# Kernel tuning notes

Hardware: AMD Instinct MI355X
Metric: run time of the kernel (lower is better)

Reference implementation:

```python
import jax, jax.numpy as jnp
import numpy as np

T = 2048
HIDDEN = 4096
NH = 32        # query heads
NKV = 8        # kv heads
G = NH // NKV  # GQA group size
D = 128        # head_dim (== v_head_dim)
ROPE_BASE = 1000000.0


def setup_inputs() -> dict:
    key = jax.random.key(0)
    ks = jax.random.split(key, 8)
    s = 0.02
    return {
        "positions": jnp.arange(T, dtype=jnp.int32),
        "hidden_states": jax.random.normal(ks[0], (T, HIDDEN), dtype=jnp.float32),
        "Wq": jax.random.normal(ks[1], (HIDDEN, NH * D), dtype=jnp.float32) * s,
        "bq": jnp.zeros((NH * D,), dtype=jnp.float32),
        "Wk": jax.random.normal(ks[2], (HIDDEN, NKV * D), dtype=jnp.float32) * s,
        "bk": jnp.zeros((NKV * D,), dtype=jnp.float32),
        "Wv": jax.random.normal(ks[3], (HIDDEN, NKV * D), dtype=jnp.float32) * s,
        "bv": jnp.zeros((NKV * D,), dtype=jnp.float32),
        "Wo": jax.random.normal(ks[4], (NH * D, HIDDEN), dtype=jnp.float32) * s,
    }


def _rope(positions, x):
    # neox-style rotary, full rotary_dim = D
    half = D // 2
    inv_freq = 1.0 / (ROPE_BASE ** (jnp.arange(0, half, dtype=jnp.float32) / half))
    freqs = positions.astype(jnp.float32)[:, None] * inv_freq[None, :]  # [T, half]
    cos = jnp.cos(freqs)[:, None, :]  # [T, 1, half]
    sin = jnp.sin(freqs)[:, None, :]
    x1, x2 = x[..., :half], x[..., half:]
    return jnp.concatenate([x1 * cos - x2 * sin, x2 * cos + x1 * sin], axis=-1)


def reference(positions, hidden_states, Wq, bq, Wk, bk, Wv, bv, Wo):
    q = (hidden_states @ Wq + bq).reshape(T, NH, D)
    k = (hidden_states @ Wk + bk).reshape(T, NKV, D)
    v = (hidden_states @ Wv + bv).reshape(T, NKV, D)
    q = _rope(positions, q)
    k = _rope(positions, k)

    scale = D ** -0.5
    qg = q.reshape(T, NKV, G, D)
    # scores: [NKV, G, T(query), S(key)]
    scores = jnp.einsum("tkgd,skd->kgts", qg, k) * scale
    causal = positions[:, None] >= positions[None, :]  # [T, S]
    scores = jnp.where(causal[None, None, :, :], scores, jnp.finfo(scores.dtype).min)
    probs = jax.nn.softmax(scores, axis=-1)
    attn = jnp.einsum("kgts,skd->tkgd", probs, v).reshape(T, NH * D)

    output = attn @ Wo
    kv_fused = jnp.stack([k, v], axis=0)  # [2, T, NKV, D]
    return output, kv_fused
```

## Files before the change

kernel.cpp:

```cpp
#include <hip/hip_runtime.h>
#include <stdint.h>

#define T_SEQ 2048
#define HIDDEN_DIM 4096
#define NH 32
#define NKV 8
#define HD 128
#define QKV_N 6144

typedef unsigned short u16;
typedef __attribute__((__ext_vector_type__(8))) __bf16 bf16x8;
typedef __attribute__((__ext_vector_type__(4))) float f32x4;

__device__ __forceinline__ float exp2_fast(float x) {
    return __builtin_amdgcn_exp2f(x);
}

__device__ __forceinline__ u16 f2bf(float f) {
    union { float f; unsigned u; } x; x.f = f;
    unsigned u = x.u;
    unsigned r = u + 0x7FFFu + ((u >> 16) & 1u);
    return (u16)(r >> 16);
}
__device__ __forceinline__ float bf2f(u16 h) {
    union { unsigned u; float f; } x; x.u = ((unsigned)h) << 16;
    return x.f;
}

__device__ __forceinline__ void gl_lds16(const u16* g, u16* l) {
    __builtin_amdgcn_global_load_lds((__attribute__((address_space(1))) void*)g,
                                     (__attribute__((address_space(3))) void*)l,
                                     16, 0, 0);
}

#define BAR()                                  \
    {                                          \
        asm volatile("" ::: "memory");         \
        __builtin_amdgcn_s_barrier();          \
        asm volatile("" ::: "memory");         \
    }

__global__ __launch_bounds__(256) void cast_f32_bf16(const float* __restrict__ in,
                                                     u16* __restrict__ out, int n4) {
    int i = blockIdx.x * 256 + threadIdx.x;
    if (i < n4) {
        float4 v = ((const float4*)in)[i];
        uint2 o;
        o.x = (unsigned)f2bf(v.x) | ((unsigned)f2bf(v.y) << 16);
        o.y = (unsigned)f2bf(v.z) | ((unsigned)f2bf(v.w) << 16);
        ((uint2*)out)[i] = o;
    }
}

__global__ __launch_bounds__(256) void transpose_cast(const float* __restrict__ W,
                                                      u16* __restrict__ Wt, int R, int C) {
    __shared__ float tile[32][33];
    int c0 = blockIdx.x * 32, r0 = blockIdx.y * 32;
    int tx = threadIdx.x & 31;
    int ty = threadIdx.x >> 5;
#pragma unroll
    for (int i = 0; i < 32; i += 8)
        tile[ty + i][tx] = W[(size_t)(r0 + ty + i) * C + c0 + tx];
    __syncthreads();
#pragma unroll
    for (int i = 0; i < 32; i += 8)
        Wt[(size_t)(c0 + ty + i) * R + r0 + tx] = f2bf(tile[tx][ty + i]);
}

__global__ __launch_bounds__(256) void concat_bias(const float* __restrict__ bq,
                                                   const float* __restrict__ bk,
                                                   const float* __restrict__ bv,
                                                   float* __restrict__ out) {
    int i = blockIdx.x * 256 + threadIdx.x;
    if (i < 4096) out[i] = bq[i];
    else if (i < 5120) out[i] = bk[i - 4096];
    else if (i < 6144) out[i] = bv[i - 5120];
}

template <int BF16_OUT, int HAS_BIAS>
__global__ __launch_bounds__(256) void gemm_bt(const u16* __restrict__ A,
                                               const u16* __restrict__ Bt,
                                               const float* __restrict__ bias,
                                               void* __restrict__ Cv,
                                               int M, int N, int K) {
    __shared__ alignas(16) u16 As[128 * 32];
    __shared__ alignas(16) u16 Bs[128 * 32];
    const int tid = threadIdx.x;
    const int wave = tid >> 6;
    const int lane = tid & 63;
    const int l15 = lane & 15;
    const int quad = lane >> 4;
    const int m0 = blockIdx.y * 128;
    const int n0 = blockIdx.x * 128;
    const int wm = (wave >> 1) * 64;
    const int wn = (wave & 1) * 64;

    f32x4 acc[4][4] = {};

    const u16* Ag = A + (size_t)(m0 + wave * 32 + (lane >> 2)) * K + (lane & 3) * 8;
    const u16* Bg = Bt + (size_t)(n0 + wave * 32 + (lane >> 2)) * K + (lane & 3) * 8;
    u16* Al = &As[wave * 32 * 32];
    u16* Bl = &Bs[wave * 32 * 32];

    for (int k0 = 0; k0 < K; k0 += 32) {
        __syncthreads();
        gl_lds16(Ag + k0, Al);
        gl_lds16(Ag + k0 + (size_t)16 * K, Al + 16 * 32);
        gl_lds16(Bg + k0, Bl);
        gl_lds16(Bg + k0 + (size_t)16 * K, Bl + 16 * 32);
        __syncthreads();
        bf16x8 af[4], bfr[4];
#pragma unroll
        for (int i = 0; i < 4; ++i)
            af[i] = *(const bf16x8*)&As[(wm + i * 16 + l15) * 32 + quad * 8];
#pragma unroll
        for (int i = 0; i < 4; ++i)
            bfr[i] = *(const bf16x8*)&Bs[(wn + i * 16 + l15) * 32 + quad * 8];
#pragma unroll
        for (int i = 0; i < 4; ++i)
#pragma unroll
            for (int j = 0; j < 4; ++j)
                acc[i][j] = __builtin_amdgcn_mfma_f32_16x16x32_bf16(af[i], bfr[j], acc[i][j], 0, 0, 0);
    }

#pragma unroll
    for (int i = 0; i < 4; ++i)
#pragma unroll
        for (int j = 0; j < 4; ++j)
#pragma unroll
            for (int r = 0; r < 4; ++r) {
                int row = m0 + wm + i * 16 + quad * 4 + r;
                int col = n0 + wn + j * 16 + l15;
                float v = acc[i][j][r];
                if (HAS_BIAS) v += bias[col];
                if (BF16_OUT) ((u16*)Cv)[(size_t)row * N + col] = f2bf(v);
                else ((float*)Cv)[(size_t)row * N + col] = v;
            }
}

#define KSTEP(S, SLOT, STG, VMW)                                                            \
    {                                                                                       \
        bf16x8 bf0_[4], af_[4];                                                             \
        _Pragma("unroll") for (int n = 0; n < 4; ++n)                                       \
            bf0_[n] = *(const bf16x8*)&Bs[SLOT][boff[n]];                                   \
        _Pragma("unroll") for (int m = 0; m < 4; ++m)                                       \
            af_[m] = *(const bf16x8*)&As[SLOT][aoff[m]];                                    \
        if (STG) {                                                                          \
            gl_lds16(Ast + (size_t)((S) + 3) * 32, &As[((SLOT) + 3) & 3][ldsS0]);           \
            gl_lds16(Ast + (size_t)((S) + 3) * 32 + rowK128, &As[((SLOT) + 3) & 3][ldsS1]); \
        }                                                                                   \
        BAR();                                                                              \
        __builtin_amdgcn_s_setprio(1);                                                      \
        _Pragma("unroll") for (int m = 0; m < 4; ++m)                                       \
            _Pragma("unroll") for (int n = 0; n < 4; ++n)                                   \
                acc[m][n] = __builtin_amdgcn_mfma_f32_16x16x32_bf16(af_[m], bf0_[n],        \
                                                                    acc[m][n], 0, 0, 0);    \
        __builtin_amdgcn_s_setprio(0);                                                      \
        BAR();                                                                              \
        _Pragma("unroll") for (int m = 0; m < 4; ++m)                                       \
            af_[m] = *(const bf16x8*)&As[SLOT][aoff[4 + m]];                                \
        if (STG) {                                                                          \
            gl_lds16(Bst + (size_t)((S) + 3) * 32, &Bs[((SLOT) + 3) & 3][ldsS0]);           \
            gl_lds16(Bst + (size_t)((S) + 3) * 32 + rowK128, &Bs[((SLOT) + 3) & 3][ldsS1]); \
        }                                                                                   \
        BAR();                                                                              \
        __builtin_amdgcn_s_setprio(1);                                                      \
        _Pragma("unroll") for (int m = 0; m < 4; ++m)                                       \
            _Pragma("unroll") for (int n = 0; n < 4; ++n)                                   \
                acc[4 + m][n] = __builtin_amdgcn_mfma_f32_16x16x32_bf16(af_[m], bf0_[n],    \
                                                                        acc[4 + m][n],      \
                                                                        0, 0, 0);           \
        __builtin_amdgcn_s_setprio(0);                                                      \
        asm volatile("s_waitcnt vmcnt(" #VMW ")" ::: "memory");                             \
        BAR();                                                                              \
    }

template <int BF16_OUT, int HAS_BIAS>
__global__ __launch_bounds__(512, 2) void gemm256(const u16* __restrict__ A,
                                                  const u16* __restrict__ Bt,
                                                  const float* __restrict__ bias,
                                                  void* __restrict__ Cv,
                                                  int M, int N, int K) {
    __shared__ alignas(16) u16 As[4][256 * 32];
    __shared__ alignas(16) u16 Bs[4][256 * 32];
    const int tid = threadIdx.x;
    const int wave = tid >> 6;
    const int lane = tid & 63;
    const int l15 = lane & 15;
    const int quad = lane >> 4;
    const int wr = wave >> 2;
    const int wc = wave & 3;

    const int nbx = N >> 8;
    const int q8 = (int)gridDim.x >> 3;
    const int wg = blockIdx.x;
    const int swz = (wg & 7) * q8 + (wg >> 3);
    const int m0 = (swz / nbx) * 256;
    const int n0 = (swz % nbx) * 256;

    const int srow = tid >> 2;
    const int schunk = (tid & 3) ^ ((tid >> 3) & 3);
    const u16* Ast = A + (size_t)(m0 + srow) * K + schunk * 8;
    const u16* Bst = Bt + (size_t)(n0 + srow) * K + schunk * 8;
    const size_t rowK128 = (size_t)128 * K;
    const int ldsS0 = wave * 512;
    const int ldsS1 = 4096 + wave * 512;

    int aoff[8], boff[4];
#pragma unroll
    for (int m = 0; m < 8; ++m) {
        int row = wr * 128 + m * 16 + l15;
        aoff[m] = row * 32 + ((quad ^ ((row >> 1) & 3)) << 3);
    }
#pragma unroll
    for (int n = 0; n < 4; ++n) {
        int row = wc * 64 + n * 16 + l15;
        boff[n] = row * 32 + ((quad ^ ((row >> 1) & 3)) << 3);
    }

    f32x4 acc[8][4] = {};
    const int NS = K >> 5;

#pragma unroll
    for (int s = 0; s < 3; ++s) {
        gl_lds16(Ast + (size_t)s * 32, &As[s][ldsS0]);
        gl_lds16(Ast + (size_t)s * 32 + rowK128, &As[s][ldsS1]);
        gl_lds16(Bst + (size_t)s * 32, &Bs[s][ldsS0]);
        gl_lds16(Bst + (size_t)s * 32 + rowK128, &Bs[s][ldsS1]);
    }
    asm volatile("s_waitcnt vmcnt(8)" ::: "memory");
    BAR();

#pragma unroll 1
    for (int s = 0; s < NS - 4; s += 4) {
        KSTEP(s, 0, 1, 4)
        KSTEP(s + 1, 1, 1, 4)
        KSTEP(s + 2, 2, 1, 4)
        KSTEP(s + 3, 3, 1, 4)
    }
    {
        const int s = NS - 4;
        KSTEP(s, 0, 1, 4)
        KSTEP(s + 1, 1, 0, 4)
        KSTEP(s + 2, 2, 0, 0)
        KSTEP(s + 3, 3, 0, 0)
    }

#pragma unroll
    for (int m = 0; m < 8; ++m) {
        const int row = m0 + wr * 128 + m * 16 + quad * 4;
#pragma unroll
        for (int n = 0; n < 4; ++n) {
            const int col = n0 + wc * 64 + n * 16 + l15;
            float b = HAS_BIAS ? bias[col] : 0.f;
#pragma unroll
            for (int r = 0; r < 4; ++r) {
                float v = acc[m][n][r] + b;
                if (BF16_OUT) ((u16*)Cv)[(size_t)(row + r) * N + col] = f2bf(v);
                else ((float*)Cv)[(size_t)(row + r) * N + col] = v;
            }
        }
    }
}

__global__ __launch_bounds__(256) void rope_kernel(const int* __restrict__ positions,
                                                   const u16* __restrict__ qkv,
                                                   u16* __restrict__ qh,
                                                   u16* __restrict__ kh,
                                                   u16* __restrict__ vt,
                                                   float* __restrict__ kv_out) {
    const int t = blockIdx.x;
    const float pos = (float)positions[t];
    const size_t rowbase = (size_t)t * QKV_N;
    const float nlog = -13.815510557964274f / 64.f;
    const float KZ = 0.08838834764831845f * 1.4426950408889634f;
    for (int col = threadIdx.x; col < QKV_N; col += 256) {
        if (col < 4096) {
            int hh = col >> 7, d = col & 127, j = d & 63;
            float ang = pos * __expf((float)j * nlog);
            float cs = cosf(ang), sn = sinf(ang);
            size_t base = rowbase + (size_t)(col & ~127);
            float x1 = bf2f(qkv[base + j]);
            float x2 = bf2f(qkv[base + 64 + j]);
            float v = (d < 64) ? (x1 * cs - x2 * sn) : (x2 * cs + x1 * sn);
            qh[((size_t)hh * T_SEQ + t) * HD + d] = f2bf(v * KZ);
        } else if (col < 5120) {
            int lc = col - 4096, hh = lc >> 7, d = lc & 127, j = d & 63;
            float ang = pos * __expf((float)j * nlog);
            float cs = cosf(ang), sn = sinf(ang);
            size_t base = rowbase + 4096 + (size_t)hh * 128;
            float x1 = bf2f(qkv[base + j]);
            float x2 = bf2f(qkv[base + 64 + j]);
            float v = (d < 64) ? (x1 * cs - x2 * sn) : (x2 * cs + x1 * sn);
            kh[((size_t)hh * T_SEQ + t) * HD + d] = f2bf(v);
            kv_out[((size_t)t * NKV + hh) * HD + d] = v;
        } else {
            int lc = col - 5120, hh = lc >> 7, d = lc & 127;
            float v = bf2f(qkv[rowbase + 5120 + (size_t)hh * 128 + d]);
            vt[((size_t)hh * HD + d) * T_SEQ + t] = f2bf(v);
            kv_out[(((size_t)T_SEQ + t) * NKV + hh) * HD + d] = v;
        }
    }
}

#define KS_STRIDE 136
#define VS_STRIDE 72
#define PS_STRIDE 72

__global__ __launch_bounds__(256) void attn_kernel(const u16* __restrict__ Qh,
                                                   const u16* __restrict__ Kh,
                                                   const u16* __restrict__ Vt,
                                                   u16* __restrict__ attn_out) {
    __shared__ alignas(16) u16 Ks[64 * KS_STRIDE];
    __shared__ alignas(16) u16 Vs[128 * VS_STRIDE];
    __shared__ alignas(16) u16 Ps[4][32 * PS_STRIDE];

    const int h = blockIdx.y;
    const int qb = (gridDim.x - 1) - blockIdx.x;
    const int tid = threadIdx.x;
    const int wave = tid >> 6;
    const int lane = tid & 63;
    const int l15 = lane & 15;
    const int quad = lane >> 4;
    const int kvh = h >> 2;
    const int wrow0 = qb * 128 + wave * 32;

    const u16* Qp = Qh + ((size_t)h * T_SEQ + wrow0) * HD;
    const u16* Kp = Kh + (size_t)kvh * T_SEQ * HD;
    const u16* Vp = Vt + (size_t)kvh * HD * T_SEQ;

    bf16x8 aQ[2][4];
#pragma unroll
    for (int i = 0; i < 2; ++i)
#pragma unroll
        for (int kb = 0; kb < 4; ++kb)
            aQ[i][kb] = *(const bf16x8*)&Qp[(size_t)(i * 16 + l15) * HD + kb * 32 + quad * 8];

    bf16x8 ones;
#pragma unroll
    for (int z = 0; z < 8; ++z) ones[z] = (__bf16)1.0f;

    f32x4 acc[2][8] = {};
    f32x4 accl[2] = {};

    const int n_tiles = 2 * qb + 2;

    const int krow = tid >> 4;
    const int kcol = (tid & 15) * 8;
    const int vrow = tid >> 3;
    const int vcol = (tid & 7) * 8;

#pragma unroll 1
    for (int t = 0; t < n_tiles; ++t) {
        const int s0 = t * 64;
        __syncthreads();
#pragma unroll
        for (int rep = 0; rep < 4; ++rep) {
            int r = krow + rep * 16;
            *(uint4*)&Ks[r * KS_STRIDE + kcol] =
                *(const uint4*)&Kp[(size_t)(s0 + r) * HD + kcol];
        }
#pragma unroll
        for (int rep = 0; rep < 4; ++rep) {
            int d = vrow + rep * 32;
            *(uint4*)&Vs[d * VS_STRIDE + vcol] =
                *(const uint4*)&Vp[(size_t)d * T_SEQ + s0 + vcol];
        }
        __syncthreads();

        if (s0 <= wrow0 + 31) {
            f32x4 sc[2][4];
#pragma unroll
            for (int j = 0; j < 4; ++j) {
                f32x4 sa = {}, sb = {};
#pragma unroll
                for (int kb = 0; kb < 4; ++kb) {
                    bf16x8 bK = *(const bf16x8*)&Ks[(j * 16 + l15) * KS_STRIDE + kb * 32 + quad * 8];
                    sa = __builtin_amdgcn_mfma_f32_16x16x32_bf16(aQ[0][kb], bK, sa, 0, 0, 0);
                    sb = __builtin_amdgcn_mfma_f32_16x16x32_bf16(aQ[1][kb], bK, sb, 0, 0, 0);
                }
                sc[0][j] = sa;
                sc[1][j] = sb;
            }
#pragma unroll
            for (int i = 0; i < 2; ++i)
#pragma unroll
                for (int r = 0; r < 4; ++r) {
                    int t_idx = wrow0 + i * 16 + quad * 4 + r;
#pragma unroll
                    for (int j = 0; j < 4; ++j) {
                        int s_idx = s0 + j * 16 + l15;
                        float z = (s_idx > t_idx) ? -1e30f : sc[i][j][r];
                        float p = exp2_fast(z);
                        Ps[wave][(i * 16 + quad * 4 + r) * PS_STRIDE + j * 16 + l15] = f2bf(p);
                    }
                }
            bf16x8 aP[2][2];
#pragma unroll
            for (int i = 0; i < 2; ++i)
#pragma unroll
                for (int k2 = 0; k2 < 2; ++k2)
                    aP[i][k2] = *(const bf16x8*)&Ps[wave][(i * 16 + l15) * PS_STRIDE + k2 * 32 + quad * 8];
#pragma unroll
            for (int o = 0; o < 8; ++o) {
                bf16x8 bV0 = *(const bf16x8*)&Vs[(o * 16 + l15) * VS_STRIDE + quad * 8];
                bf16x8 bV1 = *(const bf16x8*)&Vs[(o * 16 + l15) * VS_STRIDE + 32 + quad * 8];
#pragma unroll
                for (int i = 0; i < 2; ++i) {
                    acc[i][o] = __builtin_amdgcn_mfma_f32_16x16x32_bf16(aP[i][0], bV0, acc[i][o], 0, 0, 0);
                    acc[i][o] = __builtin_amdgcn_mfma_f32_16x16x32_bf16(aP[i][1], bV1, acc[i][o], 0, 0, 0);
                }
            }
#pragma unroll
            for (int i = 0; i < 2; ++i) {
                accl[i] = __builtin_amdgcn_mfma_f32_16x16x32_bf16(aP[i][0], ones, accl[i], 0, 0, 0);
                accl[i] = __builtin_amdgcn_mfma_f32_16x16x32_bf16(aP[i][1], ones, accl[i], 0, 0, 0);
            }
        }
    }

#pragma unroll
    for (int i = 0; i < 2; ++i)
#pragma unroll
        for (int r = 0; r < 4; ++r) {
            float inv = 1.f / accl[i][r];
            int t_idx = wrow0 + i * 16 + quad * 4 + r;
#pragma unroll
            for (int o = 0; o < 8; ++o)
                attn_out[(size_t)t_idx * (NH * HD) + h * HD + o * 16 + l15] =
                    f2bf(acc[i][o][r] * inv);
        }
}

extern "C" void kernel_launch(void* const* d_in, const int* in_sizes, int n_in,
                              void* d_out, int out_size, void* d_ws, size_t ws_size,
                              hipStream_t stream) {
    const int* positions = (const int*)d_in[0];
    const float* hidden = (const float*)d_in[1];
    const float* Wq = (const float*)d_in[2];
    const float* bq = (const float*)d_in[3];
    const float* Wk = (const float*)d_in[4];
    const float* bk = (const float*)d_in[5];
    const float* Wv = (const float*)d_in[6];
    const float* bv = (const float*)d_in[7];
    const float* Wo = (const float*)d_in[8];

    char* ws = (char*)d_ws;
    u16* hs_bf   = (u16*)(ws + 0);
    u16* attnbuf = (u16*)(ws + 0);
    u16* wqkvT   = (u16*)(ws + 16777216);
    u16* woT     = (u16*)(ws + 16777216);
    u16* qkvbuf  = (u16*)(ws + 67108864);
    u16* qbuf    = (u16*)(ws + 92274688);
    u16* kbuf    = (u16*)(ws + 109051904);
    u16* vtbuf   = (u16*)(ws + 113246208);
    float* biasb = (float*)(ws + 117440512);

    float* out0 = (float*)d_out;
    float* kvout = out0 + (size_t)T_SEQ * HIDDEN_DIM;

    cast_f32_bf16<<<dim3((T_SEQ * HIDDEN_DIM / 4 + 255) / 256), dim3(256), 0, stream>>>(
        hidden, hs_bf, T_SEQ * HIDDEN_DIM / 4);
    transpose_cast<<<dim3(128, 128), dim3(256), 0, stream>>>(Wq, wqkvT, HIDDEN_DIM, 4096);
    transpose_cast<<<dim3(32, 128), dim3(256), 0, stream>>>(Wk, wqkvT + (size_t)4096 * HIDDEN_DIM, HIDDEN_DIM, 1024);
    transpose_cast<<<dim3(32, 128), dim3(256), 0, stream>>>(Wv, wqkvT + (size_t)5120 * HIDDEN_DIM, HIDDEN_DIM, 1024);
    concat_bias<<<dim3(24), dim3(256), 0, stream>>>(bq, bk, bv, biasb);

    gemm256<1, 1><<<dim3((T_SEQ / 256) * (QKV_N / 256)), dim3(512), 0, stream>>>(
        hs_bf, wqkvT, biasb, qkvbuf, T_SEQ, QKV_N, HIDDEN_DIM);

    transpose_cast<<<dim3(128, 128), dim3(256), 0, stream>>>(Wo, woT, NH * HD, HIDDEN_DIM);

    rope_kernel<<<dim3(T_SEQ), dim3(256), 0, stream>>>(positions, qkvbuf, qbuf, kbuf, vtbuf, kvout);

    attn_kernel<<<dim3(16, NH), dim3(256), 0, stream>>>(qbuf, kbuf, vtbuf, attnbuf);

    gemm_bt<0, 0><<<dim3(HIDDEN_DIM / 128, T_SEQ / 128), dim3(256), 0, stream>>>(
        attnbuf, woT, nullptr, out0, T_SEQ, HIDDEN_DIM, NH * HD);
}
```

Measured before the change: 564.2 us.

## Use 256x192 QKV GEMM tiles and zigzag attention block ordering

The QKV projection GEMM tile changes from 256x256 to 256x192, so the grid grows from 192 to 256 workgroups and matches the 256 CUs more evenly. B staging is reworked so half the threads load the extra 64 rows, and the vmcnt waits are adjusted to match. Attention query blocks are now launched in a zigzag order, reversed for half of the heads, to balance causal work across the grid. The smaller tile lowers per-block arithmetic intensity and changes the load-wait bookkeeping, which risks pipeline stalls.

```diff
diff --git a/kernel.cpp b/kernel.cpp
--- a/kernel.cpp
+++ b/kernel.cpp
@@ -138,41 +138,42 @@
             }
 }
 
-#define KSTEP(S, SLOT, STG, VMW)                                                            \
-    {                                                                                       \
-        bf16x8 bf0_[4], af_[4];                                                             \
-        _Pragma("unroll") for (int n = 0; n < 4; ++n)                                       \
-            bf0_[n] = *(const bf16x8*)&Bs[SLOT][boff[n]];                                   \
-        _Pragma("unroll") for (int m = 0; m < 4; ++m)                                       \
-            af_[m] = *(const bf16x8*)&As[SLOT][aoff[m]];                                    \
-        if (STG) {                                                                          \
-            gl_lds16(Ast + (size_t)((S) + 3) * 32, &As[((SLOT) + 3) & 3][ldsS0]);           \
-            gl_lds16(Ast + (size_t)((S) + 3) * 32 + rowK128, &As[((SLOT) + 3) & 3][ldsS1]); \
-        }                                                                                   \
-        BAR();                                                                              \
-        __builtin_amdgcn_s_setprio(1);                                                      \
-        _Pragma("unroll") for (int m = 0; m < 4; ++m)                                       \
-            _Pragma("unroll") for (int n = 0; n < 4; ++n)                                   \
-                acc[m][n] = __builtin_amdgcn_mfma_f32_16x16x32_bf16(af_[m], bf0_[n],        \
-                                                                    acc[m][n], 0, 0, 0);    \
-        __builtin_amdgcn_s_setprio(0);                                                      \
-        BAR();                                                                              \
-        _Pragma("unroll") for (int m = 0; m < 4; ++m)                                       \
-            af_[m] = *(const bf16x8*)&As[SLOT][aoff[4 + m]];                                \
-        if (STG) {                                                                          \
-            gl_lds16(Bst + (size_t)((S) + 3) * 32, &Bs[((SLOT) + 3) & 3][ldsS0]);           \
-            gl_lds16(Bst + (size_t)((S) + 3) * 32 + rowK128, &Bs[((SLOT) + 3) & 3][ldsS1]); \
-        }                                                                                   \
-        BAR();                                                                              \
-        __builtin_amdgcn_s_setprio(1);                                                      \
-        _Pragma("unroll") for (int m = 0; m < 4; ++m)                                       \
-            _Pragma("unroll") for (int n = 0; n < 4; ++n)                                   \
-                acc[4 + m][n] = __builtin_amdgcn_mfma_f32_16x16x32_bf16(af_[m], bf0_[n],    \
-                                                                        acc[4 + m][n],      \
-                                                                        0, 0, 0);           \
-        __builtin_amdgcn_s_setprio(0);                                                      \
-        asm volatile("s_waitcnt vmcnt(" #VMW ")" ::: "memory");                             \
-        BAR();                                                                              \
+#define KSTEP(S, SLOT, STG, VMW)                                                             \
+    {                                                                                        \
+        bf16x8 bf_[3], af_[4];                                                               \
+        _Pragma("unroll") for (int n = 0; n < 3; ++n)                                        \
+            bf_[n] = *(const bf16x8*)&Bs[SLOT][boff[n]];                                     \
+        _Pragma("unroll") for (int m = 0; m < 4; ++m)                                        \
+            af_[m] = *(const bf16x8*)&As[SLOT][aoff[m]];                                     \
+        if (STG) {                                                                           \
+            gl_lds16(Ast + (size_t)((S) + 3) * 32, &As[((SLOT) + 3) & 3][ldsS0]);            \
+            gl_lds16(Ast + (size_t)((S) + 3) * 32 + rowK128, &As[((SLOT) + 3) & 3][ldsS1]);  \
+        }                                                                                    \
+        BAR();                                                                               \
+        __builtin_amdgcn_s_setprio(1);                                                       \
+        _Pragma("unroll") for (int m = 0; m < 4; ++m)                                        \
+            _Pragma("unroll") for (int n = 0; n < 3; ++n)                                    \
+                acc[m][n] = __builtin_amdgcn_mfma_f32_16x16x32_bf16(af_[m], bf_[n],          \
+                                                                    acc[m][n], 0, 0, 0);     \
+        __builtin_amdgcn_s_setprio(0);                                                       \
+        BAR();                                                                               \
+        _Pragma("unroll") for (int m = 0; m < 4; ++m)                                        \
+            af_[m] = *(const bf16x8*)&As[SLOT][aoff[4 + m]];                                 \
+        if (STG) {                                                                           \
+            gl_lds16(Bst + (size_t)((S) + 3) * 32, &Bs[((SLOT) + 3) & 3][ldsB0]);            \
+            if (tid < 256)                                                                   \
+                gl_lds16(BstH + (size_t)((S) + 3) * 32, &Bs[((SLOT) + 3) & 3][ldsB2]);       \
+        }                                                                                    \
+        BAR();                                                                               \
+        __builtin_amdgcn_s_setprio(1);                                                       \
+        _Pragma("unroll") for (int m = 0; m < 4; ++m)                                        \
+            _Pragma("unroll") for (int n = 0; n < 3; ++n)                                    \
+                acc[4 + m][n] = __builtin_amdgcn_mfma_f32_16x16x32_bf16(af_[m], bf_[n],      \
+                                                                        acc[4 + m][n],       \
+                                                                        0, 0, 0);            \
+        __builtin_amdgcn_s_setprio(0);                                                       \
+        asm volatile("s_waitcnt vmcnt(" #VMW ")" ::: "memory");                              \
+        BAR();                                                                               \
     }
 
 template <int BF16_OUT, int HAS_BIAS>
@@ -182,7 +183,7 @@
                                                   void* __restrict__ Cv,
                                                   int M, int N, int K) {
     __shared__ alignas(16) u16 As[4][256 * 32];
-    __shared__ alignas(16) u16 Bs[4][256 * 32];
+    __shared__ alignas(16) u16 Bs[4][192 * 32];
     const int tid = threadIdx.x;
     const int wave = tid >> 6;
     const int lane = tid & 63;
@@ -191,57 +192,60 @@
     const int wr = wave >> 2;
     const int wc = wave & 3;
 
-    const int nbx = N >> 8;
+    const int nbn = N / 192;
     const int q8 = (int)gridDim.x >> 3;
     const int wg = blockIdx.x;
     const int swz = (wg & 7) * q8 + (wg >> 3);
-    const int m0 = (swz / nbx) * 256;
-    const int n0 = (swz % nbx) * 256;
+    const int m0 = (swz / nbn) * 256;
+    const int n0 = (swz % nbn) * 192;
 
     const int srow = tid >> 2;
     const int schunk = (tid & 3) ^ ((tid >> 3) & 3);
     const u16* Ast = A + (size_t)(m0 + srow) * K + schunk * 8;
     const u16* Bst = Bt + (size_t)(n0 + srow) * K + schunk * 8;
+    const u16* BstH = Bt + (size_t)(n0 + 128 + srow) * K + schunk * 8;
     const size_t rowK128 = (size_t)128 * K;
     const int ldsS0 = wave * 512;
     const int ldsS1 = 4096 + wave * 512;
-
-    int aoff[8], boff[4];
+    const int ldsB0 = wave * 512;
+    const int ldsB2 = 4096 + wave * 512;
+
+    int aoff[8], boff[3];
 #pragma unroll
     for (int m = 0; m < 8; ++m) {
         int row = wr * 128 + m * 16 + l15;
         aoff[m] = row * 32 + ((quad ^ ((row >> 1) & 3)) << 3);
     }
 #pragma unroll
-    for (int n = 0; n < 4; ++n) {
-        int row = wc * 64 + n * 16 + l15;
+    for (int n = 0; n < 3; ++n) {
+        int row = wc * 48 + n * 16 + l15;
         boff[n] = row * 32 + ((quad ^ ((row >> 1) & 3)) << 3);
     }
 
-    f32x4 acc[8][4] = {};
+    f32x4 acc[8][3] = {};
     const int NS = K >> 5;
 
 #pragma unroll
     for (int s = 0; s < 3; ++s) {
         gl_lds16(Ast + (size_t)s * 32, &As[s][ldsS0]);
         gl_lds16(Ast + (size_t)s * 32 + rowK128, &As[s][ldsS1]);
-        gl_lds16(Bst + (size_t)s * 32, &Bs[s][ldsS0]);
-        gl_lds16(Bst + (size_t)s * 32 + rowK128, &Bs[s][ldsS1]);
-    }
-    asm volatile("s_waitcnt vmcnt(8)" ::: "memory");
+        gl_lds16(Bst + (size_t)s * 32, &Bs[s][ldsB0]);
+        if (tid < 256) gl_lds16(BstH + (size_t)s * 32, &Bs[s][ldsB2]);
+    }
+    asm volatile("s_waitcnt vmcnt(6)" ::: "memory");
     BAR();
 
 #pragma unroll 1
     for (int s = 0; s < NS - 4; s += 4) {
-        KSTEP(s, 0, 1, 4)
-        KSTEP(s + 1, 1, 1, 4)
-        KSTEP(s + 2, 2, 1, 4)
-        KSTEP(s + 3, 3, 1, 4)
+        KSTEP(s, 0, 1, 6)
+        KSTEP(s + 1, 1, 1, 6)
+        KSTEP(s + 2, 2, 1, 6)
+        KSTEP(s + 3, 3, 1, 6)
     }
     {
         const int s = NS - 4;
-        KSTEP(s, 0, 1, 4)
-        KSTEP(s + 1, 1, 0, 4)
+        KSTEP(s, 0, 1, 6)
+        KSTEP(s + 1, 1, 0, 6)
         KSTEP(s + 2, 2, 0, 0)
         KSTEP(s + 3, 3, 0, 0)
     }
@@ -250,8 +254,8 @@
     for (int m = 0; m < 8; ++m) {
         const int row = m0 + wr * 128 + m * 16 + quad * 4;
 #pragma unroll
-        for (int n = 0; n < 4; ++n) {
-            const int col = n0 + wc * 64 + n * 16 + l15;
+        for (int n = 0; n < 3; ++n) {
+            const int col = n0 + wc * 48 + n * 16 + l15;
             float b = HAS_BIAS ? bias[col] : 0.f;
 #pragma unroll
             for (int r = 0; r < 4; ++r) {
@@ -316,7 +320,9 @@
     __shared__ alignas(16) u16 Ps[4][32 * PS_STRIDE];
 
     const int h = blockIdx.y;
-    const int qb = (gridDim.x - 1) - blockIdx.x;
+    const int x = blockIdx.x;
+    const int zig = (x & 1) ? ((x - 1) >> 1) : (15 - (x >> 1));
+    const int qb = (h < 16) ? zig : (15 - zig);
     const int tid = threadIdx.x;
     const int wave = tid >> 6;
     const int lane = tid & 63;
@@ -466,7 +472,7 @@
     transpose_cast<<<dim3(32, 128), dim3(256), 0, stream>>>(Wv, wqkvT + (size_t)5120 * HIDDEN_DIM, HIDDEN_DIM, 1024);
     concat_bias<<<dim3(24), dim3(256), 0, stream>>>(bq, bk, bv, biasb);
 
-    gemm256<1, 1><<<dim3((T_SEQ / 256) * (QKV_N / 256)), dim3(512), 0, stream>>>(
+    gemm256<1, 1><<<dim3((T_SEQ / 256) * (QKV_N / 192)), dim3(512), 0, stream>>>(
         hs_bf, wqkvT, biasb, qkvbuf, T_SEQ, QKV_N, HIDDEN_DIM);
 
     transpose_cast<<<dim3(128, 128), dim3(256), 0, stream>>>(Wo, woT, NH * HD, HIDDEN_DIM);
```

New measurement: 544.4 us. 3.5% less time.
